# Optimization experiments

Hardware: AMD Instinct MI355X
Metric: run time of the kernel (lower is better)

The kernel has to match this reference:

```python
import jax, jax.numpy as jnp
import numpy as np

N, D_IN, D_OUT, E = 8192, 2048, 8192, 8


def setup_inputs() -> dict:
    key = jax.random.key(0)
    k1, k2, k3 = jax.random.split(key, 3)
    x = jax.random.normal(k1, (N, D_IN), dtype=jnp.float32)
    # packed weight layout [E, in, out] (pack() pretransposes [E,out,in] -> [E,in,out])
    weight = jax.random.normal(k2, (E, D_IN, D_OUT), dtype=jnp.float32) * (1.0 / np.sqrt(D_IN))
    indices = jax.random.randint(k3, (N,), 0, E, dtype=jnp.int32)
    return {"x": x, "weight": weight, "indices": indices}


def reference(x, weight, indices):
    # gather_mm: out[n] = x[n] @ weight[indices[n]]  -> [N, D_OUT]
    # Avoid materializing weight[indices] ([N, in, out]); instead loop over the
    # small fixed expert count, masking tokens routed to each expert.
    n_experts = weight.shape[0]
    out = jnp.zeros((x.shape[0], weight.shape[-1]), dtype=x.dtype)
    for e in range(n_experts):
        mask = (indices == e)[:, None]
        xe = jnp.where(mask, x, 0)          # zero out tokens not routed to e
        out = out + xe @ weight[e]           # [N, in] @ [in, out]
    return out
```

## Files before the change

kernel.cpp:

```cpp
#include <hip/hip_runtime.h>
#include <hip/hip_bf16.h>
#include <stdint.h>

#define N_TOK 8192
#define D_IN  2048
#define D_OUT 8192
#define NEXP  8
#define KST   32
#define NT2   40
#define NS2   32
#define AIMG  32768
#define X_OFF2 65536
#define X_BYTES2 ((long)NT2 * KST * AIMG)
#define W_OFF2 (X_OFF2 + X_BYTES2)
#define W_BYTES2 ((long)NEXP * NS2 * KST * AIMG)
#define WS_NEED2 ((size_t)(W_OFF2 + W_BYTES2))


typedef float  f32x4  __attribute__((ext_vector_type(4)));
typedef __bf16 bf16x8 __attribute__((ext_vector_type(8)));

__global__ void SwitchLinear_setup_kernel(const int* __restrict__ idx,
                                          int* __restrict__ ws) {
    __shared__ int cnt[NEXP], cur[NEXP];
    int t = threadIdx.x;
    if (t < NEXP) cnt[t] = 0;
    __syncthreads();
    for (int i = t; i < N_TOK; i += 256) atomicAdd(&cnt[idx[i]], 1);
    __syncthreads();
    if (t == 0) {
        int o = 0, nt = 0, nt1 = 0;
        for (int e = 0; e < NEXP; ++e) {
            cur[e] = o;
            int c = cnt[e];
            for (int r = 0; r < c; r += 256) {
                ws[8 + nt]   = e;
                ws[96 + nt]  = o + r;
                ws[192 + nt] = (c - r < 256) ? (c - r) : 256;
                ++nt;
            }
            for (int r = 0; r < c; r += 128) {
                ws[256 + nt1] = e;
                ws[328 + nt1] = o + r;
                ws[400 + nt1] = (c - r < 128) ? (c - r) : 128;
                ++nt1;
            }
            o += c;
        }
        ws[0] = nt;
        ws[4] = nt1;
    }
    __syncthreads();
    for (int i = t; i < N_TOK; i += 256) {
        int p = atomicAdd(&cur[idx[i]], 1);
        ws[512 + p] = i;
    }
}


__global__ __launch_bounds__(256) void SwitchLinear_convx_kernel(
    const float* __restrict__ x, const int* __restrict__ ws,
    char* __restrict__ wsb) {
    const int tile = blockIdx.x, kst = blockIdx.y;
    if (tile >= ws[0]) return;
    const int rs = ws[96 + tile], rows = ws[192 + tile];
    char* img = wsb + X_OFF2 + (long)(tile * KST + kst) * AIMG;
    const int t = threadIdx.x;
#pragma unroll
    for (int i = 0; i < 8; ++i) {
        int u = t + i * 256;
        int R = u >> 3, kc8 = u & 7;
        int rl = rs + (R < rows ? R : rows - 1);
        int token = ws[512 + rl];
        const float* src = x + (long)token * D_IN + kst * 64 + kc8 * 8;
        f32x4 v0 = *(const f32x4*)src;
        f32x4 v1 = *(const f32x4*)(src + 4);
        union { __bf16 hh[8]; uint4 u4; } c;
        c.hh[0] = (__bf16)v0[0]; c.hh[1] = (__bf16)v0[1];
        c.hh[2] = (__bf16)v0[2]; c.hh[3] = (__bf16)v0[3];
        c.hh[4] = (__bf16)v1[0]; c.hh[5] = (__bf16)v1[1];
        c.hh[6] = (__bf16)v1[2]; c.hh[7] = (__bf16)v1[3];
        int slot = (((R & 1) << 2) | (kc8 & 3)) ^ ((R >> 1) & 7);
        *(uint4*)(img + (kc8 >> 2) * 16384 + ((R >> 1) << 7) + (slot << 4)) = c.u4;
    }
}

__global__ __launch_bounds__(256) void SwitchLinear_convw_kernel(
    const float* __restrict__ w, char* __restrict__ wsb) {
    const int img = blockIdx.x;
    const int kst = img & 31, s = (img >> 5) & 63, e = img >> 11;
    const int y = s >> 1, hh = s & 1;
    __shared__ float tl[64 * 129];
    const float* src = w + (long)e * D_IN * D_OUT + (long)(kst * 64) * D_OUT +
                       y * 256 + hh * 128;
    const int t = threadIdx.x;
#pragma unroll
    for (int i = 0; i < 8; ++i) {
        int u = t + i * 256;
        int row = u >> 5, ch = u & 31;
        f32x4 v = *(const f32x4*)(src + (long)row * D_OUT + ch * 4);
        float* d = &tl[row * 129 + ch * 4];
        d[0] = v[0]; d[1] = v[1]; d[2] = v[2]; d[3] = v[3];
    }
    __syncthreads();
    char* dimg = wsb + W_OFF2 + (long)((e * NS2 + y) * KST + kst) * AIMG;
#pragma unroll
    for (int i = 0; i < 4; ++i) {
        int u = t + i * 256;
        int cl = u >> 3, kc8 = u & 7;
        union { __bf16 h8[8]; uint4 u4; } c;
#pragma unroll
        for (int j = 0; j < 8; ++j) c.h8[j] = (__bf16)tl[(kc8 * 8 + j) * 129 + cl];
        int cc = hh * 128 + cl;
        int slot = (((cc & 1) << 2) | (kc8 & 3)) ^ ((cc >> 1) & 7);
        *(uint4*)(dimg + (kc8 >> 2) * 16384 + ((cc >> 1) << 7) + (slot << 4)) = c.u4;
    }
}


__global__ __launch_bounds__(512, 1) void SwitchLinear_gemm_kernel(
    const char* __restrict__ wsb, const int* __restrict__ ws,
    float* __restrict__ out) {
    const int bid = blockIdx.x;
    const int lb  = (bid & 7) * ((NT2 * NS2) / 8) + (bid >> 3);
    const int tx  = lb % NT2;
    const int y   = lb / NT2;
    if (tx >= ws[0]) return;
    const int e = ws[8 + tx], rs = ws[96 + tx], rows = ws[192 + tx];

    __shared__ __align__(16) char ldsA[2][2][16384];
    __shared__ __align__(16) char ldsB[3][2][16384];

    const int t = threadIdx.x;

    const char* aImg = wsb + X_OFF2 + (long)(tx * KST) * AIMG;
    const char* bImg = wsb + W_OFF2 + (long)((e * NS2 + y) * KST) * AIMG;

    const int lane = t & 63;
    const int wid  = t >> 6;
    const int wr = wid >> 2, wc = wid & 3;
    const int lm = lane & 15, lk = lane >> 4;

    int tok[8][4];
#pragma unroll
    for (int mi = 0; mi < 8; ++mi)
#pragma unroll
        for (int j = 0; j < 4; ++j) {
            int rl = wr * 128 + mi * 16 + lk * 4 + j;
            tok[mi][j] = ws[512 + rs + (rl < rows ? rl : 0)];
        }

    f32x4 acc[8][4];
#pragma unroll
    for (int i = 0; i < 8; ++i)
#pragma unroll
        for (int j = 0; j < 4; ++j) acc[i][j] = (f32x4){0.f, 0.f, 0.f, 0.f};

    bf16x8 aa[4], bb[4];

#define STGA(ks, half, tt)                                                    \
    __builtin_amdgcn_global_load_lds(                                         \
        (const __attribute__((address_space(1))) uint32_t*)(                  \
            aImg + (long)(tt) * AIMG + (ks) * 16384 + (half) * 8192 + t * 16),\
        (__attribute__((address_space(3))) uint32_t*)(                        \
            &ldsA[(tt) & 1][ks][(half) * 8192 + t * 16]),                     \
        16, 0, 0)

#define STGB(ks, half, tt)                                                    \
    __builtin_amdgcn_global_load_lds(                                         \
        (const __attribute__((address_space(1))) uint32_t*)(                  \
            bImg + (long)(tt) * AIMG + (ks) * 16384 + (half) * 8192 + t * 16),\
        (__attribute__((address_space(3))) uint32_t*)(                        \
            &ldsB[(tt) % 3][ks][(half) * 8192 + t * 16]),                     \
        16, 0, 0)

#define SWB(r) ((((r) >> 1) << 7) + (((((((r) & 1) << 2)) | lk) ^ (((r) >> 1) & 7)) << 4))

#define LDB(pb, ks)                                                           \
    do { _Pragma("unroll")                                                    \
        for (int ni = 0; ni < 4; ++ni) {                                      \
            int cc = wc * 64 + ni * 16 + lm;                                  \
            bb[ni] = *(const bf16x8*)(&ldsB[pb][ks][SWB(cc)]);                \
        } } while (0)

#define LDA(pa, ks, mh)                                                       \
    do { _Pragma("unroll")                                                    \
        for (int q = 0; q < 4; ++q) {                                         \
            int rr = wr * 128 + (mh) * 64 + q * 16 + lm;                      \
            aa[q] = *(const bf16x8*)(&ldsA[pa][ks][SWB(rr)]);                 \
        } } while (0)

#define MFMA16(mh)                                                            \
    do { _Pragma("unroll")                                                    \
        for (int q = 0; q < 4; ++q)                                           \
            _Pragma("unroll")                                                 \
            for (int ni = 0; ni < 4; ++ni)                                    \
                acc[(mh) * 4 + q][ni] = __builtin_amdgcn_mfma_f32_16x16x32_bf16( \
                    aa[q], bb[ni], acc[(mh) * 4 + q][ni], 0, 0, 0);           \
    } while (0)

#define PH(BODY_LD, ISSUE, MH, POST)                                          \
    do {                                                                      \
        BODY_LD;                                                              \
        ISSUE;                                                                \
        __builtin_amdgcn_s_barrier();                                         \
        asm volatile("s_waitcnt lgkmcnt(0)" ::: "memory");                    \
        __builtin_amdgcn_sched_barrier(0);                                    \
        __builtin_amdgcn_s_setprio(1);                                        \
        MFMA16(MH);                                                           \
        __builtin_amdgcn_s_setprio(0);                                        \
        POST;                                                                 \
        __builtin_amdgcn_s_barrier();                                         \
    } while (0)

    STGA(0, 0, 0); STGA(0, 1, 0); STGA(1, 0, 0); STGA(1, 1, 0);
    STGB(0, 0, 0); STGB(0, 1, 0); STGB(1, 0, 0); STGB(1, 1, 0);
    STGB(0, 0, 1); STGB(0, 1, 1); STGB(1, 0, 1); STGB(1, 1, 1);
    asm volatile("s_waitcnt vmcnt(4)" ::: "memory");
    __builtin_amdgcn_s_barrier();

    for (int tt = 0; tt < KST; ++tt) {
        const int pa = tt & 1;
        const int pb = tt % 3;
        const int nxA = tt + 1;
        const int nxB = tt + 2;
        const bool iA = nxA < KST;
        const bool iB = nxB < KST;
        PH({ LDB(pb, 0); LDA(pa, 0, 0); },
           { if (iA) { STGA(0, 0, nxA); STGA(0, 1, nxA); } }, 0, ((void)0));
        PH({ LDA(pa, 0, 1); },
           { if (iA) { STGA(1, 0, nxA); STGA(1, 1, nxA); } }, 1, ((void)0));
        PH({ LDB(pb, 1); LDA(pa, 1, 0); },
           { if (iB) { STGB(0, 0, nxB); STGB(0, 1, nxB); } }, 0, ((void)0));
        PH({ LDA(pa, 1, 1); },
           { if (iB) { STGB(1, 0, nxB); STGB(1, 1, nxB); } }, 1,
           { if (tt < KST - 2)
                 asm volatile("s_waitcnt vmcnt(4)" ::: "memory");
             else if (tt == KST - 2)
                 asm volatile("s_waitcnt vmcnt(0)" ::: "memory"); });
    }

#pragma unroll
    for (int mi = 0; mi < 8; ++mi) {
#pragma unroll
        for (int j = 0; j < 4; ++j) {
            int rl = wr * 128 + mi * 16 + lk * 4 + j;
            if (rl < rows) {
                float* po = out + (long)tok[mi][j] * D_OUT + y * 256 + wc * 64 + lm;
#pragma unroll
                for (int ni = 0; ni < 4; ++ni) po[ni * 16] = acc[mi][ni][j];
            }
        }
    }
#undef STGA
#undef STGB
#undef SWB
#undef LDB
#undef LDA
#undef MFMA16
#undef PH
}


__device__ __forceinline__ int fb_a_byte(int r, int kbyte) {
    return r * 128 + (kbyte ^ ((r & 7) << 4));
}
__device__ __forceinline__ int fb_b_byte(int n, int kbyte) {
    int slot = (n ^ (n >> 2)) & 7;
    return n * 128 + (kbyte ^ (slot << 4));
}

__global__ __launch_bounds__(256, 2) void SwitchLinear_gemm_fb_kernel(
    const float* __restrict__ x, const float* __restrict__ w,
    const int* __restrict__ ws, float* __restrict__ out) {
    const int nt = ws[4];
    const int tx = blockIdx.x;
    if (tx >= nt) return;
    const int e    = ws[256 + tx];
    const int rs   = ws[328 + tx];
    const int rows = ws[400 + tx];
    const int col0 = blockIdx.y * 128;

    __shared__ __align__(16) unsigned short As[128 * 64];
    __shared__ __align__(16) unsigned short Bs[128 * 64];
    __shared__ int ord[128];

    const int t = threadIdx.x;
    if (t < 128) {
        int r = (t < rows) ? (rs + t) : rs;
        ord[t] = ws[512 + r];
    }
    __syncthreads();

    const int kq = t & 15;
    const float* pA[8];
    int rowA[8];
#pragma unroll
    for (int i = 0; i < 8; ++i) {
        int r = (t >> 4) + 16 * i;
        rowA[i] = r;
        pA[i] = x + (long)ord[r] * D_IN + kq * 4;
    }
    const float* pB[2];
    int nB[2], kbB[2];
#pragma unroll
    for (int i = 0; i < 2; ++i) {
        int u = t + 256 * i;
        int kgf = u >> 5, q = u & 31;
        kbB[i] = kgf * 4;
        nB[i]  = q * 4;
        pB[i]  = w + (long)e * D_IN * D_OUT + (long)(kgf * 4) * D_OUT + col0 + q * 4;
    }

    const int lane = t & 63;
    const int wid  = t >> 6;
    const int wr = wid >> 1, wc = wid & 1;
    const int lm = lane & 15, lk = lane >> 4;

    f32x4 acc[4][4];
#pragma unroll
    for (int i = 0; i < 4; ++i)
#pragma unroll
        for (int j = 0; j < 4; ++j) acc[i][j] = (f32x4){0.f, 0.f, 0.f, 0.f};

    for (int k0 = 0; k0 < D_IN; k0 += 64) {
#pragma unroll
        for (int i = 0; i < 8; ++i) {
            f32x4 v = *(const f32x4*)(pA[i] + k0);
            union { __bf16 h[4]; uint2 u; } c;
            c.h[0] = (__bf16)v[0]; c.h[1] = (__bf16)v[1];
            c.h[2] = (__bf16)v[2]; c.h[3] = (__bf16)v[3];
            *(uint2*)((char*)As + fb_a_byte(rowA[i], kq * 8)) = c.u;
        }
#pragma unroll
        for (int i = 0; i < 2; ++i) {
            const float* p = pB[i] + (long)k0 * D_OUT;
            f32x4 r0 = *(const f32x4*)(p);
            f32x4 r1 = *(const f32x4*)(p + D_OUT);
            f32x4 r2 = *(const f32x4*)(p + 2 * D_OUT);
            f32x4 r3 = *(const f32x4*)(p + 3 * D_OUT);
#pragma unroll
            for (int j = 0; j < 4; ++j) {
                int n = nB[i] + j;
                union { __bf16 h[4]; uint2 u; } c;
                c.h[0] = (__bf16)r0[j]; c.h[1] = (__bf16)r1[j];
                c.h[2] = (__bf16)r2[j]; c.h[3] = (__bf16)r3[j];
                *(uint2*)((char*)Bs + fb_b_byte(n, kbB[i] * 2)) = c.u;
            }
        }
        __syncthreads();
#pragma unroll
        for (int ks = 0; ks < 2; ++ks) {
            bf16x8 a[4], b[4];
            const int kbyte = ks * 64 + lk * 16;
#pragma unroll
            for (int mi = 0; mi < 4; ++mi) {
                int r = wr * 64 + mi * 16 + lm;
                a[mi] = *(const bf16x8*)((const char*)As + fb_a_byte(r, kbyte));
            }
#pragma unroll
            for (int ni = 0; ni < 4; ++ni) {
                int n = wc * 64 + ni * 16 + lm;
                b[ni] = *(const bf16x8*)((const char*)Bs + fb_b_byte(n, kbyte));
            }
#pragma unroll
            for (int mi = 0; mi < 4; ++mi)
#pragma unroll
                for (int ni = 0; ni < 4; ++ni)
                    acc[mi][ni] = __builtin_amdgcn_mfma_f32_16x16x32_bf16(
                        a[mi], b[ni], acc[mi][ni], 0, 0, 0);
        }
        __syncthreads();
    }
#pragma unroll
    for (int mi = 0; mi < 4; ++mi) {
#pragma unroll
        for (int j = 0; j < 4; ++j) {
            int rl = wr * 64 + mi * 16 + lk * 4 + j;
            if (rl < rows) {
                int token = ord[rl];
                float* po = out + (long)token * D_OUT + col0 + wc * 64 + lm;
#pragma unroll
                for (int ni = 0; ni < 4; ++ni) po[ni * 16] = acc[mi][ni][j];
            }
        }
    }
}

extern "C" void kernel_launch(void* const* d_in, const int* in_sizes, int n_in,
                              void* d_out, int out_size, void* d_ws, size_t ws_size,
                              hipStream_t stream) {
    const float* x   = (const float*)d_in[0];
    const float* w   = (const float*)d_in[1];
    const int*   idx = (const int*)d_in[2];
    float* out = (float*)d_out;
    int*   ws  = (int*)d_ws;
    char*  wsb = (char*)d_ws;

    SwitchLinear_setup_kernel<<<1, 256, 0, stream>>>(idx, ws);
    if (ws_size >= WS_NEED2) {
        SwitchLinear_convx_kernel<<<dim3(NT2, KST), 256, 0, stream>>>(x, ws, wsb);
        SwitchLinear_convw_kernel<<<NEXP * 64 * KST, 256, 0, stream>>>(w, wsb);
        SwitchLinear_gemm_kernel<<<NT2 * NS2, 512, 0, stream>>>(wsb, ws, out);
    } else {
        dim3 grid(72, 64);
        SwitchLinear_gemm_fb_kernel<<<grid, 256, 0, stream>>>(x, w, ws, out);
    }
}
```

Before: 595.5 us.

## Simplify GEMM pipeline to double-buffered B with one barrier per k-step

Cuts the B-tile LDS ring from triple to double buffering. The four per-phase barrier pairs become a single full vmcnt wait plus barrier at the end of each k-step, with A and B both prefetched one step ahead. Per-row token indices move from a 32-entry register array into a shared LDS table read only in the epilogue, which frees VGPRs. The aim is less barrier overhead and register pressure, but with prefetch depth reduced to one step, global-memory latency may be less well hidden.

New measurement: 563.9 us. 5.3% less time.

```diff
diff --git a/kernel.cpp b/kernel.cpp
--- a/kernel.cpp
+++ b/kernel.cpp
@@ -129,9 +129,11 @@
     const int e = ws[8 + tx], rs = ws[96 + tx], rows = ws[192 + tx];
 
     __shared__ __align__(16) char ldsA[2][2][16384];
-    __shared__ __align__(16) char ldsB[3][2][16384];
+    __shared__ __align__(16) char ldsB[2][2][16384];
+    __shared__ int ord[256];
 
     const int t = threadIdx.x;
+    if (t < 256) ord[t] = ws[512 + rs + (t < rows ? t : 0)];
 
     const char* aImg = wsb + X_OFF2 + (long)(tx * KST) * AIMG;
     const char* bImg = wsb + W_OFF2 + (long)((e * NS2 + y) * KST) * AIMG;
@@ -140,15 +142,6 @@
     const int wid  = t >> 6;
     const int wr = wid >> 2, wc = wid & 3;
     const int lm = lane & 15, lk = lane >> 4;
-
-    int tok[8][4];
-#pragma unroll
-    for (int mi = 0; mi < 8; ++mi)
-#pragma unroll
-        for (int j = 0; j < 4; ++j) {
-            int rl = wr * 128 + mi * 16 + lk * 4 + j;
-            tok[mi][j] = ws[512 + rs + (rl < rows ? rl : 0)];
-        }
 
     f32x4 acc[8][4];
 #pragma unroll
@@ -171,23 +164,23 @@
         (const __attribute__((address_space(1))) uint32_t*)(                  \
             bImg + (long)(tt) * AIMG + (ks) * 16384 + (half) * 8192 + t * 16),\
         (__attribute__((address_space(3))) uint32_t*)(                        \
-            &ldsB[(tt) % 3][ks][(half) * 8192 + t * 16]),                     \
+            &ldsB[(tt) & 1][ks][(half) * 8192 + t * 16]),                     \
         16, 0, 0)
 
 #define SWB(r) ((((r) >> 1) << 7) + (((((((r) & 1) << 2)) | lk) ^ (((r) >> 1) & 7)) << 4))
 
-#define LDB(pb, ks)                                                           \
+#define LDB(p, ks)                                                            \
     do { _Pragma("unroll")                                                    \
         for (int ni = 0; ni < 4; ++ni) {                                      \
             int cc = wc * 64 + ni * 16 + lm;                                  \
-            bb[ni] = *(const bf16x8*)(&ldsB[pb][ks][SWB(cc)]);                \
+            bb[ni] = *(const bf16x8*)(&ldsB[p][ks][SWB(cc)]);                 \
         } } while (0)
 
-#define LDA(pa, ks, mh)                                                       \
+#define LDA(p, ks, mh)                                                        \
     do { _Pragma("unroll")                                                    \
         for (int q = 0; q < 4; ++q) {                                         \
             int rr = wr * 128 + (mh) * 64 + q * 16 + lm;                      \
-            aa[q] = *(const bf16x8*)(&ldsA[pa][ks][SWB(rr)]);                 \
+            aa[q] = *(const bf16x8*)(&ldsA[p][ks][SWB(rr)]);                  \
         } } while (0)
 
 #define MFMA16(mh)                                                            \
@@ -199,45 +192,37 @@
                     aa[q], bb[ni], acc[(mh) * 4 + q][ni], 0, 0, 0);           \
     } while (0)
 
-#define PH(BODY_LD, ISSUE, MH, POST)                                          \
+#define PH(BODY_LD, ISSUE, MH)                                                \
     do {                                                                      \
         BODY_LD;                                                              \
         ISSUE;                                                                \
-        __builtin_amdgcn_s_barrier();                                         \
         asm volatile("s_waitcnt lgkmcnt(0)" ::: "memory");                    \
         __builtin_amdgcn_sched_barrier(0);                                    \
         __builtin_amdgcn_s_setprio(1);                                        \
         MFMA16(MH);                                                           \
         __builtin_amdgcn_s_setprio(0);                                        \
-        POST;                                                                 \
-        __builtin_amdgcn_s_barrier();                                         \
     } while (0)
 
     STGA(0, 0, 0); STGA(0, 1, 0); STGA(1, 0, 0); STGA(1, 1, 0);
     STGB(0, 0, 0); STGB(0, 1, 0); STGB(1, 0, 0); STGB(1, 1, 0);
-    STGB(0, 0, 1); STGB(0, 1, 1); STGB(1, 0, 1); STGB(1, 1, 1);
-    asm volatile("s_waitcnt vmcnt(4)" ::: "memory");
+    asm volatile("s_waitcnt vmcnt(0)" ::: "memory");
+    asm volatile("s_waitcnt lgkmcnt(0)" ::: "memory");
     __builtin_amdgcn_s_barrier();
 
     for (int tt = 0; tt < KST; ++tt) {
-        const int pa = tt & 1;
-        const int pb = tt % 3;
-        const int nxA = tt + 1;
-        const int nxB = tt + 2;
-        const bool iA = nxA < KST;
-        const bool iB = nxB < KST;
-        PH({ LDB(pb, 0); LDA(pa, 0, 0); },
-           { if (iA) { STGA(0, 0, nxA); STGA(0, 1, nxA); } }, 0, ((void)0));
-        PH({ LDA(pa, 0, 1); },
-           { if (iA) { STGA(1, 0, nxA); STGA(1, 1, nxA); } }, 1, ((void)0));
-        PH({ LDB(pb, 1); LDA(pa, 1, 0); },
-           { if (iB) { STGB(0, 0, nxB); STGB(0, 1, nxB); } }, 0, ((void)0));
-        PH({ LDA(pa, 1, 1); },
-           { if (iB) { STGB(1, 0, nxB); STGB(1, 1, nxB); } }, 1,
-           { if (tt < KST - 2)
-                 asm volatile("s_waitcnt vmcnt(4)" ::: "memory");
-             else if (tt == KST - 2)
-                 asm volatile("s_waitcnt vmcnt(0)" ::: "memory"); });
+        const int p  = tt & 1;
+        const int nx = tt + 1;
+        const bool iA = nx < KST;
+        PH({ LDB(p, 0); LDA(p, 0, 0); },
+           { if (iA) { STGA(0, 0, nx); STGA(0, 1, nx); } }, 0);
+        PH({ LDA(p, 0, 1); },
+           { if (iA) { STGA(1, 0, nx); STGA(1, 1, nx); } }, 1);
+        PH({ LDB(p, 1); LDA(p, 1, 0); },
+           { if (iA) { STGB(0, 0, nx); STGB(0, 1, nx); } }, 0);
+        PH({ LDA(p, 1, 1); },
+           { if (iA) { STGB(1, 0, nx); STGB(1, 1, nx); } }, 1);
+        asm volatile("s_waitcnt vmcnt(0)" ::: "memory");
+        __builtin_amdgcn_s_barrier();
     }
 
 #pragma unroll
@@ -246,7 +231,8 @@
         for (int j = 0; j < 4; ++j) {
             int rl = wr * 128 + mi * 16 + lk * 4 + j;
             if (rl < rows) {
-                float* po = out + (long)tok[mi][j] * D_OUT + y * 256 + wc * 64 + lm;
+                int token = ord[rl];
+                float* po = out + (long)token * D_OUT + y * 256 + wc * 64 + lm;
 #pragma unroll
                 for (int ni = 0; ni < 4; ++ni) po[ni * 16] = acc[mi][ni][j];
             }
```
